# Optimization experiments

Hardware: AMD Instinct MI355X
Metric: run time of the kernel (lower is better)

Reference implementation:

```python
import jax, jax.numpy as jnp
import numpy as np

N = 8192
K = 64
EPS = 1e-7
BN_EPS = 1e-5


def _norm(x):
    return jnp.sqrt(jnp.sum(x * x, axis=-1, keepdims=True))


def _bn(x, gamma, beta):
    # BatchNorm2d in training mode (batch statistics, biased variance)
    mu = jnp.mean(x, axis=(0, 2, 3), keepdims=True)
    var = jnp.mean((x - mu) ** 2, axis=(0, 2, 3), keepdims=True)
    return gamma.reshape(1, -1, 1, 1) * (x - mu) / jnp.sqrt(var + BN_EPS) + beta.reshape(1, -1, 1, 1)


def _conv1x1(x, w, b):
    # 1x1 conv == per-pixel linear: x [B,C,H,W], w [O,C]
    return jnp.einsum('bchw,oc->bohw', x, w) + b.reshape(1, -1, 1, 1)


def setup_inputs() -> dict:
    key = jax.random.key(0)
    ks = jax.random.split(key, 24)
    d = {}
    d['points'] = jax.random.normal(ks[0], (1, N, 3), jnp.float32)
    # graph_conv weights (torch code re-draws these every forward; here fixed params)
    lim0 = float(np.sqrt(6.0 / (4 + 64)))
    d['gw0'] = jax.random.uniform(ks[1], (4, 64), jnp.float32, -lim0, lim0)
    lim = float(np.sqrt(6.0 / (64 + 64)))
    for i in range(1, 5):
        d[f'gw{i}'] = jax.random.uniform(ks[1 + i], (64, 64), jnp.float32, -lim, lim)
    # mlp_1: 4->64->128, mlp_2: 192->256->1024 (1x1 convs + BN)
    d['c1w'] = jax.random.normal(ks[6], (64, 4), jnp.float32) * 0.1
    d['c1b'] = jnp.zeros((64,), jnp.float32)
    d['bn1g'] = jnp.ones((64,), jnp.float32)
    d['bn1b'] = jnp.zeros((64,), jnp.float32)
    d['c2w'] = jax.random.normal(ks[7], (128, 64), jnp.float32) * 0.1
    d['c2b'] = jnp.zeros((128,), jnp.float32)
    d['bn2g'] = jnp.ones((128,), jnp.float32)
    d['bn2b'] = jnp.zeros((128,), jnp.float32)
    d['c3w'] = jax.random.normal(ks[8], (256, 192), jnp.float32) * 0.05
    d['c3b'] = jnp.zeros((256,), jnp.float32)
    d['bn3g'] = jnp.ones((256,), jnp.float32)
    d['bn3b'] = jnp.zeros((256,), jnp.float32)
    d['c4w'] = jax.random.normal(ks[9], (1024, 256), jnp.float32) * 0.05
    d['c4b'] = jnp.zeros((1024,), jnp.float32)
    d['bn4g'] = jnp.ones((1024,), jnp.float32)
    d['bn4b'] = jnp.zeros((1024,), jnp.float32)
    return d


def _knn_search(points, k):
    # pairwise squared distances via ||a||^2 - 2ab + ||b||^2
    r = jnp.sum(points * points, axis=-1, keepdims=True)          # [1,N,1]
    dis = r - 2.0 * jnp.einsum('bnd,bmd->bnm', points, points) + jnp.swapaxes(r, 1, 2)
    _, idx = jax.lax.top_k(-dis, k)                                # [1,N,K]
    knn_pts = jax.vmap(lambda p, i: p[i])(points, idx)             # [1,N,K,3]
    return knn_pts


def _proj_knn(knn_pts):
    b, n, k, _ = knn_pts.shape
    pc = knn_pts - knn_pts[:, :, :1, :]                            # center on first neighbor (self)
    vn = jnp.sqrt(jnp.sum(pc * pc, axis=-1))                       # [1,N,K]
    id1 = jnp.argmax(vn, axis=-1)                                  # farthest neighbor
    a1 = jnp.take_along_axis(pc, jnp.broadcast_to(id1[:, :, None, None], (b, n, 1, 3)), axis=2)[:, :, 0, :]
    a1 = a1 / (_norm(a1) + EPS)
    a2 = jnp.mean(pc, axis=2)
    a2 = a2 / (_norm(a2) + EPS)
    a3 = a1 + 1.5 * a2
    a3 = a3 / (_norm(a3) + EPS)
    den = _norm(pc) + EPS                                          # [1,N,K,1]
    f1 = jnp.sum(pc * a1[:, :, None, :], axis=-1, keepdims=True) / den
    f2 = jnp.sum(pc * a2[:, :, None, :], axis=-1, keepdims=True) / den
    f3 = jnp.sum(pc * a3[:, :, None, :], axis=-1, keepdims=True) / den
    return jnp.concatenate([f1, f2, f3, vn[..., None]], axis=-1)   # [1,N,K,4]


def _proj_points(points):
    b, n, _ = points.shape
    vn = jnp.sqrt(jnp.sum(points * points, axis=-1))               # [1,N]
    i1 = jnp.argmax(vn, axis=-1)
    i2 = jnp.argmin(vn, axis=-1)
    a1 = jnp.take_along_axis(points, jnp.broadcast_to(i1[:, None, None], (b, 1, 3)), axis=1)[:, 0, :]
    a1 = a1 / (_norm(a1) + EPS)
    a2 = jnp.take_along_axis(points, jnp.broadcast_to(i2[:, None, None], (b, 1, 3)), axis=1)[:, 0, :]
    a2 = a2 / (_norm(a2) + EPS)
    a3 = a1 + 1.5 * a2
    a3 = a3 / (_norm(a3) + EPS)
    den = _norm(points) + EPS                                      # [1,N,1]
    f1 = jnp.sum(points * a1[:, None, :], axis=-1, keepdims=True) / den
    f2 = jnp.sum(points * a2[:, None, :], axis=-1, keepdims=True) / den
    f3 = jnp.sum(points * a3[:, None, :], axis=-1, keepdims=True) / den
    return jnp.concatenate([f1, f2, f3, vn[..., None]], axis=-1)   # [1,N,4]


def reference(points, gw0, gw1, gw2, gw3, gw4,
              c1w, c1b, bn1g, bn1b, c2w, c2b, bn2g, bn2b,
              c3w, c3b, bn3g, bn3b, c4w, c4b, bn4g, bn4b):
    n = points.shape[1]
    # upper branch: KNN -> rotation-invariant local feats -> 5-layer MLP -> max over K
    knn_pts = _knn_search(points, K)
    feat_up = _proj_knn(knn_pts)                                   # [1,N,K,4]
    x = feat_up.reshape(-1, 4)
    for w in (gw0, gw1, gw2, gw3, gw4):
        x = jax.nn.relu(x @ w)
    x = x.reshape(1, n, K, 64)
    emb_up = jnp.max(x, axis=2, keepdims=True)                     # [1,N,1,64]
    emb_up = emb_up.reshape(1, 64, n, 1)                           # raw view (reshape), as in torch
    # lower branch: global rotation-invariant feats -> mlp_1
    feat_down = _proj_points(points)                               # [1,N,4]
    emb_down = feat_down.reshape(1, 4, n, 1)                       # raw view (reshape), as in torch
    h = jax.nn.relu(_bn(_conv1x1(emb_down, c1w, c1b), bn1g, bn1b))
    h = jax.nn.relu(_bn(_conv1x1(h, c2w, c2b), bn2g, bn2b))        # [1,128,N,1]
    emb = jnp.concatenate([emb_up, h], axis=1)                     # [1,192,N,1]
    out = jax.nn.relu(_bn(_conv1x1(emb, c3w, c3b), bn3g, bn3b))
    out = jax.nn.relu(_bn(_conv1x1(out, c4w, c4b), bn4g, bn4b))    # [1,1024,N,1]
    return out
```

## Files before the change

### kernel.cpp

```cpp
#include <hip/hip_runtime.h>
#include <hip/hip_bf16.h>

#define NPTS 8192
#define KNN 64
#define EPSF 1e-7f

#define OFF_P4      0
#define OFF_STATS   32768
#define OFF_AVEC    36000
#define OFF_PART    36012
#define OFF_FEATDN  36864
#define OFF_WT1     69632
#define OFF_GWT     69888
#define OFF_BW2     79104
#define OFF_BW3     83200
#define OFF_BW4     107776
#define OFF_XB1     238848
#define OFF_XB3     500992
#define OFF_XB4     1287424
#define OFF_Y1      2336000
#define OFF_Y2      2860288
#define OFF_Y3      3908864
#define OFF_FEATUP  6006016

#define OFF_P4S     OFF_Y1
#define OFF_TBND    (OFF_Y1 + 32768)
#define OFF_BCNT    (OFF_Y1 + 33024)
#define OFF_BOFS    (OFF_Y1 + 33088)
#define OFF_BFIL    (OFF_Y1 + 33156)

typedef __bf16 bf16x8 __attribute__((ext_vector_type(8)));
typedef float  f32x4  __attribute__((ext_vector_type(4)));

__device__ __forceinline__ unsigned f2u(float f) {
    unsigned u = __float_as_uint(f);
    return ((int)u >= 0) ? (u | 0x80000000u) : ~u;
}
__device__ __forceinline__ float key_to_f(unsigned long long k) {
    unsigned v = (unsigned)(k >> 32);
    unsigned ob = (v & 0x80000000u) ? (v ^ 0x80000000u) : ~v;
    return __uint_as_float(ob);
}
__device__ __forceinline__ unsigned short f2bf(float x) {
    unsigned u = __float_as_uint(x);
    unsigned r = (u + 0x7FFFu + ((u >> 16) & 1u)) >> 16;
    return (unsigned short)r;
}
__device__ __forceinline__ unsigned long long u64min(unsigned long long a, unsigned long long b){ return a < b ? a : b; }
__device__ __forceinline__ unsigned long long u64max(unsigned long long a, unsigned long long b){ return a < b ? b : a; }

__device__ __forceinline__ unsigned long long sort_merge(
    unsigned long long key, unsigned long long cur, int lane)
{
    #pragma unroll
    for (int k = 2; k <= 64; k <<= 1) {
        #pragma unroll
        for (int j = k >> 1; j > 0; j >>= 1) {
            unsigned long long o = __shfl_xor(key, j);
            bool up = ((lane & k) == 0);
            bool lower = ((lane & j) == 0);
            key = (lower == up) ? u64min(key, o) : u64max(key, o);
        }
    }
    unsigned long long rev = __shfl(key, 63 - lane);
    unsigned long long m = u64min(cur, rev);
    #pragma unroll
    for (int j = 32; j > 0; j >>= 1) {
        unsigned long long o = __shfl_xor(m, j);
        m = ((lane & j) == 0) ? u64min(m, o) : u64max(m, o);
    }
    return m;
}

__device__ __forceinline__ int xbin(float x) {
    int b = (int)((x + 4.5f) * (64.0f / 9.0f));
    return min(63, max(0, b));
}

__global__ __launch_bounds__(256) void prep_a_kernel(
    const float* __restrict__ points, float* __restrict__ ws)
{
    const int n = blockIdx.x * 256 + threadIdx.x;
    float x = points[3*n+0], y = points[3*n+1], z = points[3*n+2];
    float rr = x*x + y*y + z*z;
    ((float4*)(ws + OFF_P4))[n] = make_float4(x, y, z, rr);
    atomicAdd((int*)(ws + OFF_BCNT) + xbin(x), 1);
    float vn = sqrtf(rr);
    unsigned b = __float_as_uint(vn);
    unsigned long long mxk = ((unsigned long long)b << 32) | (unsigned long long)(0xFFFFFFFFu - (unsigned)n);
    unsigned long long mnk = ((unsigned long long)b << 32) | (unsigned long long)(unsigned)n;
    for (int j = 32; j > 0; j >>= 1) {
        mxk = u64max(mxk, __shfl_xor(mxk, j));
        mnk = u64min(mnk, __shfl_xor(mnk, j));
    }
    __shared__ unsigned long long smx[4], smn[4];
    int wid = threadIdx.x >> 6;
    if ((threadIdx.x & 63) == 0) { smx[wid] = mxk; smn[wid] = mnk; }
    __syncthreads();
    if (threadIdx.x == 0) {
        unsigned long long MX = 0ull, MN = ~0ull;
        for (int i = 0; i < 4; ++i) { MX = u64max(MX, smx[i]); MN = u64min(MN, smn[i]); }
        unsigned long long* parts = (unsigned long long*)(ws + OFF_PART);
        parts[2*blockIdx.x + 0] = MX;
        parts[2*blockIdx.x + 1] = MN;
    }
}

__global__ __launch_bounds__(64) void prep_b_kernel(
    const float* __restrict__ points, float* __restrict__ ws)
{
    const int lane = threadIdx.x;
    const unsigned long long* parts = (const unsigned long long*)(ws + OFF_PART);
    unsigned long long mxk = (lane < 32) ? parts[2*lane + 0] : 0ull;
    unsigned long long mnk = (lane < 32) ? parts[2*lane + 1] : ~0ull;
    for (int j = 32; j > 0; j >>= 1) {
        mxk = u64max(mxk, __shfl_xor(mxk, j));
        mnk = u64min(mnk, __shfl_xor(mnk, j));
    }
    if (lane == 0) {
        int i1 = (int)(0xFFFFFFFFu - (unsigned)(mxk & 0xFFFFFFFFu));
        int i2 = (int)(unsigned)(mnk & 0xFFFFFFFFu);
        float a1x = points[3*i1+0], a1y = points[3*i1+1], a1z = points[3*i1+2];
        float n1 = sqrtf(a1x*a1x + a1y*a1y + a1z*a1z) + EPSF;
        a1x /= n1; a1y /= n1; a1z /= n1;
        float a2x = points[3*i2+0], a2y = points[3*i2+1], a2z = points[3*i2+2];
        float n2 = sqrtf(a2x*a2x + a2y*a2y + a2z*a2z) + EPSF;
        a2x /= n2; a2y /= n2; a2z /= n2;
        float a3x = a1x + 1.5f*a2x, a3y = a1y + 1.5f*a2y, a3z = a1z + 1.5f*a2z;
        float n3 = sqrtf(a3x*a3x + a3y*a3y + a3z*a3z) + EPSF;
        a3x /= n3; a3y /= n3; a3z /= n3;
        float* av = ws + OFF_AVEC;
        av[0]=a1x; av[1]=a1y; av[2]=a1z;
        av[3]=a2x; av[4]=a2y; av[5]=a2z;
        av[6]=a3x; av[7]=a3y; av[8]=a3z;
    }
    if (lane == 1) {
        const int* cnt = (const int*)(ws + OFF_BCNT);
        int* ofs = (int*)(ws + OFF_BOFS);
        int* fil = (int*)(ws + OFF_BFIL);
        int acc = 0;
        for (int i = 0; i < 64; ++i) { ofs[i] = acc; fil[i] = acc; acc += cnt[i]; }
        ofs[64] = acc;
    }
}

__global__ __launch_bounds__(256) void prep_cs_kernel(float* __restrict__ ws)
{
    const int n = blockIdx.x * 256 + threadIdx.x;
    const float* av = ws + OFF_AVEC;
    float4 v = ((const float4*)(ws + OFF_P4))[n];
    float vn = sqrtf(v.w);
    float den = vn + EPSF;
    float f1 = (v.x*av[0] + v.y*av[1] + v.z*av[2]) / den;
    float f2 = (v.x*av[3] + v.y*av[4] + v.z*av[5]) / den;
    float f3 = (v.x*av[6] + v.y*av[7] + v.z*av[8]) / den;
    ((float4*)(ws + OFF_FEATDN))[n] = make_float4(f1, f2, f3, vn);

    int pos = atomicAdd((int*)(ws + OFF_BFIL) + xbin(v.x), 1);
    ((float4*)(ws + OFF_P4S))[pos] = make_float4(v.x, v.y, v.z, __int_as_float(n));
}

__global__ __launch_bounds__(256) void bounds_kernel(float* __restrict__ ws)
{
    const int w = blockIdx.x, tid = threadIdx.x;
    const float4* p = (const float4*)(ws + OFF_P4S);
    float mn = 1e30f, mx = -1e30f;
    #pragma unroll
    for (int i = 0; i < 4; ++i) {
        float x = p[w*1024 + tid + i*256].x;
        mn = fminf(mn, x); mx = fmaxf(mx, x);
    }
    for (int j = 32; j > 0; j >>= 1) {
        mn = fminf(mn, __shfl_xor(mn, j));
        mx = fmaxf(mx, __shfl_xor(mx, j));
    }
    __shared__ float smn[4], smx[4];
    int wid = tid >> 6;
    if ((tid & 63) == 0) { smn[wid] = mn; smx[wid] = mx; }
    __syncthreads();
    if (tid == 0) {
        float MN = fminf(fminf(smn[0], smn[1]), fminf(smn[2], smn[3]));
        float MX = fmaxf(fmaxf(smx[0], smx[1]), fmaxf(smx[2], smx[3]));
        ws[OFF_TBND + 2*w] = MN;
        ws[OFF_TBND + 2*w + 1] = MX;
    }
}

__global__ __launch_bounds__(256) void wt_kernel(
    const float* __restrict__ c1w, const float* __restrict__ c2w,
    const float* __restrict__ c3w, const float* __restrict__ c4w,
    const float* __restrict__ gw0, const float* __restrict__ gw1,
    const float* __restrict__ gw2, const float* __restrict__ gw3,
    const float* __restrict__ gw4,
    float* __restrict__ ws)
{
    const int t = blockIdx.x * 256 + threadIdx.x;
    const int T = gridDim.x * 256;
    for (int m = t; m < 2944; m += T) ws[OFF_STATS + m] = 0.f;
    for (int m = t; m < 64; m += T) ((int*)(ws + OFF_BCNT))[m] = 0;
    for (int m = t; m < 64*4; m += T) { int o = m >> 2, c = m & 3; ws[OFF_WT1 + c*64 + o] = c1w[m]; }

    unsigned short* bw2 = (unsigned short*)(ws + OFF_BW2);
    for (int m = t; m < 128*64; m += T)   bw2[m] = f2bf(c2w[m]);
    unsigned short* bw3 = (unsigned short*)(ws + OFF_BW3);
    for (int m = t; m < 256*192; m += T)  bw3[m] = f2bf(c3w[m]);
    unsigned short* bw4 = (unsigned short*)(ws + OFF_BW4);
    for (int m = t; m < 1024*256; m += T) bw4[m] = f2bf(c4w[m]);

    unsigned short* gwt = (unsigned short*)(ws + OFF_GWT);
    for (int m = t; m < 2048; m += T) {
        int o = m >> 5, i = m & 31;
        gwt[m] = (i < 4) ? f2bf(gw0[i*64 + o]) : (unsigned short)0;
    }
    const float* gsrc[4] = {gw1, gw2, gw3, gw4};
    for (int l = 0; l < 4; ++l) {
        const float* g = gsrc[l];
        unsigned short* dst = gwt + 2048 + l*4096;
        for (int m = t; m < 4096; m += T) { int o = m >> 6, i = m & 63; dst[m] = f2bf(g[i*64 + o]); }
    }
}

__global__ __launch_bounds__(512) void knn_feat_kernel(
    const float4* __restrict__ p4,
    const float4* __restrict__ p4s,
    const float* __restrict__ wbnd,
    float4* __restrict__ feat_up)
{
    __shared__ __align__(16) float4 stage[1024];
    __shared__ unsigned long long queue[8][2][128];
    __shared__ float sb[16], pmx[8], pmn[8];
    __shared__ int voteL, voteR, nextT;

    const int lane = threadIdx.x & 63;
    const int wid  = threadIdx.x >> 6;
    if (threadIdx.x < 16) sb[threadIdx.x] = wbnd[threadIdx.x];
    __syncthreads();
    if (threadIdx.x == 0) {
        float m = -1e30f;
        for (int w = 0; w < 8; ++w) { m = fmaxf(m, sb[2*w+1]); pmx[w] = m; }
        float n = 1e30f;
        for (int w = 7; w >= 0; --w) { n = fminf(n, sb[2*w]); pmn[w] = n; }
    }

    const int s0 = blockIdx.x * 16 + wid * 2;
    float4 qa = p4s[s0];
    float4 qb = p4s[s0 + 1];
    const int qi0 = __float_as_int(qa.w), qi1 = __float_as_int(qb.w);
    qa.w = fmaf(qa.x, qa.x, fmaf(qa.y, qa.y, qa.z * qa.z));
    qb.w = fmaf(qb.x, qb.x, fmaf(qb.y, qb.y, qb.z * qb.z));

    unsigned long long* Q0 = queue[wid][0];
    unsigned long long* Q1 = queue[wid][1];
    unsigned long long cur0 = ~0ull, cur1 = ~0ull;
    float kthd0 = __builtin_inff(), kthd1 = __builtin_inff();
    int qc0 = 0, qc1 = 0;

    const int w0 = blockIdx.x >> 6;
    int L = w0, R = w0, t = w0;

    for (;;) {
        __syncthreads();
        for (int i = threadIdx.x; i < 1024; i += 512) stage[i] = p4s[t*1024 + i];
        if (threadIdx.x == 0) { voteL = 0; voteR = 0; }
        __syncthreads();

        float wmn = sb[2*t], wmx = sb[2*t+1];
        float ga = fmaxf(fmaxf(qa.x - wmx, wmn - qa.x), 0.f);
        float gb = fmaxf(fmaxf(qb.x - wmx, wmn - qb.x), 0.f);
        if (!((ga*ga > kthd0) && (gb*gb > kthd1))) {
            #pragma unroll 2
            for (int sub = 0; sub < 1024; sub += 64) {
                float4 cd = stage[sub + lane];
                int ci = __float_as_int(cd.w);
                float cr = fmaf(cd.x, cd.x, fmaf(cd.y, cd.y, cd.z * cd.z));
                float dot0 = fmaf(qa.x, cd.x, fmaf(qa.y, cd.y, qa.z * cd.z));
                float d0   = fmaf(-2.f, dot0, qa.w) + cr;
                float dot1 = fmaf(qb.x, cd.x, fmaf(qb.y, cd.y, qb.z * cd.z));
                float d1   = fmaf(-2.f, dot1, qb.w) + cr;
                bool p0 = d0 <= kthd0, p1 = d1 <= kthd1;
                unsigned long long m0 = __ballot(p0);
                unsigned long long m1 = __ballot(p1);
                if (m0) {
                    int prefix = __builtin_amdgcn_mbcnt_hi((unsigned)(m0 >> 32),
                                  __builtin_amdgcn_mbcnt_lo((unsigned)m0, 0));
                    if (p0) Q0[qc0 + prefix] = ((unsigned long long)f2u(d0) << 32)
                                             | (unsigned long long)(unsigned)ci;
                    qc0 += __popcll(m0);
                    if (qc0 >= 64) {
                        qc0 -= 64;
                        cur0 = sort_merge(Q0[qc0 + lane], cur0, lane);
                        kthd0 = key_to_f(__shfl(cur0, 63));
                    }
                }
                if (m1) {
                    int prefix = __builtin_amdgcn_mbcnt_hi((unsigned)(m1 >> 32),
                                  __builtin_amdgcn_mbcnt_lo((unsigned)m1, 0));
                    if (p1) Q1[qc1 + prefix] = ((unsigned long long)f2u(d1) << 32)
                                             | (unsigned long long)(unsigned)ci;
                    qc1 += __popcll(m1);
                    if (qc1 >= 64) {
                        qc1 -= 64;
                        cur1 = sort_merge(Q1[qc1 + lane], cur1, lane);
                        kthd1 = key_to_f(__shfl(cur1, 63));
                    }
                }
            }
        }

        if (lane == 0) {
            bool needL = false, needR = false;
            if (L > 0) {
                float p = pmx[L-1];
                float g0 = qa.x - p, g1 = qb.x - p;
                bool st0 = (g0 > 0.f) && (g0*g0 > kthd0);
                bool st1 = (g1 > 0.f) && (g1*g1 > kthd1);
                needL = !(st0 && st1);
            }
            if (R < 7) {
                float p = pmn[R+1];
                float g0 = p - qa.x, g1 = p - qb.x;
                bool st0 = (g0 > 0.f) && (g0*g0 > kthd0);
                bool st1 = (g1 > 0.f) && (g1*g1 > kthd1);
                needR = !(st0 && st1);
            }
            if (needL) atomicOr(&voteL, 1);
            if (needR) atomicOr(&voteR, 1);
        }
        __syncthreads();
        if (threadIdx.x == 0) {
            bool cL = (voteL != 0) && (L > 0);
            bool cR = (voteR != 0) && (R < 7);
            int nt = -1;
            if (cL && cR) nt = ((w0 - (L-1)) <= ((R+1) - w0)) ? (L-1) : (R+1);
            else if (cL) nt = L - 1;
            else if (cR) nt = R + 1;
            nextT = nt;
        }
        __syncthreads();
        t = nextT;
        if (t < 0) break;
        if (t < L) L = t; else R = t;
    }

    cur0 = sort_merge((lane < qc0) ? Q0[lane] : ~0ull, cur0, lane);
    cur1 = sort_merge((lane < qc1) ? Q1[lane] : ~0ull, cur1, lane);

    #pragma unroll 1
    for (int j = 0; j < 2; ++j) {
        unsigned long long cur = j ? cur1 : cur0;
        const int q = j ? qi1 : qi0;
        int nidx = (int)(unsigned)(cur & 0xFFFFFFFFu);
        float4 np = p4[nidx];
        float ox = __shfl(np.x, 0), oy = __shfl(np.y, 0), oz = __shfl(np.z, 0);
        float pcx = np.x - ox, pcy = np.y - oy, pcz = np.z - oz;
        float vn = sqrtf(pcx*pcx + pcy*pcy + pcz*pcz);

        unsigned long long ak = ((unsigned long long)__float_as_uint(vn) << 32)
                              | (unsigned long long)(unsigned)(63 - lane);
        for (int s = 32; s > 0; s >>= 1) ak = u64max(ak, __shfl_xor(ak, s));
        int id1 = 63 - (int)(unsigned)(ak & 0xFFFFFFFFu);

        float a1x = __shfl(pcx, id1), a1y = __shfl(pcy, id1), a1z = __shfl(pcz, id1);
        float n1 = sqrtf(a1x*a1x + a1y*a1y + a1z*a1z) + EPSF;
        a1x /= n1; a1y /= n1; a1z /= n1;

        float sx = pcx, sy = pcy, sz = pcz;
        for (int s = 32; s > 0; s >>= 1) {
            sx += __shfl_xor(sx, s); sy += __shfl_xor(sy, s); sz += __shfl_xor(sz, s);
        }
        float a2x = sx * (1.f/64.f), a2y = sy * (1.f/64.f), a2z = sz * (1.f/64.f);
        float n2 = sqrtf(a2x*a2x + a2y*a2y + a2z*a2z) + EPSF;
        a2x /= n2; a2y /= n2; a2z /= n2;

        float a3x = a1x + 1.5f*a2x, a3y = a1y + 1.5f*a2y, a3z = a1z + 1.5f*a2z;
        float n3 = sqrtf(a3x*a3x + a3y*a3y + a3z*a3z) + EPSF;
        a3x /= n3; a3y /= n3; a3z /= n3;

        float den = vn + EPSF;
        float f1 = (pcx*a1x + pcy*a1y + pcz*a1z) / den;
        float f2 = (pcx*a2x + pcy*a2y + pcz*a2z) / den;
        float f3 = (pcx*a3x + pcy*a3y + pcz*a3z) / den;
        feat_up[q*64 + lane] = make_float4(f1, f2, f3, vn);
    }
}

#define BROW 72
__global__ __launch_bounds__(256) void mlp_kernel(
    const float4* __restrict__ feat_up,
    const unsigned short* __restrict__ gwt,
    unsigned short* __restrict__ xb3)
{
    __shared__ __align__(16) unsigned short Blds[4][64 * BROW];
    const int lane = threadIdx.x & 63;
    const int wid  = threadIdx.x >> 6;
    const int q = blockIdx.x * 4 + wid;
    const int c = lane & 15, g = lane >> 4;
    unsigned short* B = Blds[wid];

    {
        float4 f = feat_up[q*64 + lane];
        uint2 p0;
        p0.x = (unsigned)f2bf(f.x) | ((unsigned)f2bf(f.y) << 16);
        p0.y = (unsigned)f2bf(f.z) | ((unsigned)f2bf(f.w) << 16);
        *(uint2*)&B[lane*BROW] = p0;
        *(uint2*)&B[lane*BROW + 4] = make_uint2(0, 0);
        uint4 z4 = make_uint4(0, 0, 0, 0);
        *(uint4*)&B[lane*BROW + 8]  = z4;
        *(uint4*)&B[lane*BROW + 16] = z4;
        *(uint4*)&B[lane*BROW + 24] = z4;
    }

    const unsigned short* Wl[5] = {gwt, gwt + 2048, gwt + 6144, gwt + 10240, gwt + 14336};
    f32x4 acc[4][4];

    for (int layer = 0; layer < 5; ++layer) {
        const int wstride = (layer == 0) ? 32 : 64;
        const int nks = (layer == 0) ? 1 : 2;
        #pragma unroll
        for (int mb = 0; mb < 4; ++mb)
            #pragma unroll
            for (int nb = 0; nb < 4; ++nb)
                acc[mb][nb] = (f32x4){0.f, 0.f, 0.f, 0.f};

        for (int ks = 0; ks < nks; ++ks) {
            bf16x8 af[4], bf[4];
            #pragma unroll
            for (int mb = 0; mb < 4; ++mb)
                af[mb] = *(const bf16x8*)(Wl[layer] + (mb*16 + c)*wstride + ks*32 + g*8);
            #pragma unroll
            for (int nb = 0; nb < 4; ++nb)
                bf[nb] = *(const bf16x8*)&B[(nb*16 + c)*BROW + ks*32 + g*8];
            #pragma unroll
            for (int mb = 0; mb < 4; ++mb)
                #pragma unroll
                for (int nb = 0; nb < 4; ++nb)
                    acc[mb][nb] = __builtin_amdgcn_mfma_f32_16x16x32_bf16(af[mb], bf[nb], acc[mb][nb], 0, 0, 0);
        }

        if (layer < 4) {
            #pragma unroll
            for (int mb = 0; mb < 4; ++mb) {
                #pragma unroll
                for (int nb = 0; nb < 4; ++nb) {
                    f32x4 a = acc[mb][nb];
                    float r0 = fmaxf(a[0], 0.f), r1 = fmaxf(a[1], 0.f);
                    float r2 = fmaxf(a[2], 0.f), r3 = fmaxf(a[3], 0.f);
                    uint2 pw;
                    pw.x = (unsigned)f2bf(r0) | ((unsigned)f2bf(r1) << 16);
                    pw.y = (unsigned)f2bf(r2) | ((unsigned)f2bf(r3) << 16);
                    *(uint2*)&B[(nb*16 + c)*BROW + mb*16 + g*4] = pw;
                }
            }
        }
    }

    const int cc = q >> 7;
    const int pbase = (q & 127) << 6;
    #pragma unroll
    for (int mb = 0; mb < 4; ++mb) {
        float v[4];
        #pragma unroll
        for (int r = 0; r < 4; ++r)
            v[r] = fmaxf(fmaxf(fmaxf(acc[mb][0][r], acc[mb][1][r]),
                               fmaxf(acc[mb][2][r], acc[mb][3][r])), 0.f);
        #pragma unroll
        for (int mask = 1; mask <= 8; mask <<= 1)
            #pragma unroll
            for (int r = 0; r < 4; ++r)
                v[r] = fmaxf(v[r], __shfl_xor(v[r], mask));
        if (c == 0) {
            #pragma unroll
            for (int r = 0; r < 4; ++r) {
                const int f = mb*16 + g*4 + r;
                xb3[(size_t)(pbase + f) * 192 + cc] = f2bf(v[r]);
            }
        }
    }
}

__global__ __launch_bounds__(256) void conv1_kernel(
    const float* __restrict__ x, const float* __restrict__ wt,
    const float* __restrict__ bias, float* __restrict__ y,
    float* __restrict__ stout)
{
    const int tid = threadIdx.x;
    const int p  = blockIdx.x * 256 + tid;
    const int o0 = blockIdx.y * 32;
    float acc[32];
    #pragma unroll
    for (int u = 0; u < 32; ++u) acc[u] = bias[o0 + u];
    #pragma unroll
    for (int c = 0; c < 4; ++c) {
        float xv = x[c * NPTS + p];
        const float* wr = wt + c * 64 + o0;
        #pragma unroll
        for (int u = 0; u < 32; ++u) acc[u] = fmaf(xv, wr[u], acc[u]);
    }
    #pragma unroll
    for (int u = 0; u < 32; ++u) y[(o0 + u) * NPTS + p] = acc[u];

    __shared__ float ps[4][32], pss[4][32];
    const int wid = tid >> 6, lane = tid & 63;
    #pragma unroll
    for (int u = 0; u < 32; ++u) {
        float s = acc[u], ss = acc[u] * acc[u];
        for (int j = 32; j > 0; j >>= 1) { s += __shfl_xor(s, j); ss += __shfl_xor(ss, j); }
        if (lane == 0) { ps[wid][u] = s; pss[wid][u] = ss; }
    }
    __syncthreads();
    if (tid < 32) {
        float S  = ps[0][tid] + ps[1][tid] + ps[2][tid] + ps[3][tid];
        float SS = pss[0][tid] + pss[1][tid] + pss[2][tid] + pss[3][tid];
        atomicAdd(&stout[o0 + tid], S);
        atomicAdd(&stout[64 + o0 + tid], SS);
    }
}

__global__ __launch_bounds__(256) void bnpack_kernel(
    const float* __restrict__ y, const float* __restrict__ st,
    const float* __restrict__ gam, const float* __restrict__ bet,
    int C, int stride, int coff, unsigned short* __restrict__ xb)
{
    __shared__ float sc[256], sh[256];
    __shared__ __align__(16) unsigned short tile[64][264];
    const int tid = threadIdx.x;
    for (int cc = tid; cc < C; cc += 256) {
        float mu  = st[cc] * (1.f / 8192.f);
        float var = st[C + cc] * (1.f / 8192.f) - mu * mu;
        float s = gam[cc] / sqrtf(var + 1e-5f);
        sc[cc] = s; sh[cc] = bet[cc] - mu * s;
    }
    __syncthreads();
    const int pl = tid & 63, g = tid >> 6;
    const int p = blockIdx.x * 64 + pl;
    for (int c0 = g * 8; c0 < C; c0 += 32) {
        unsigned pk[4];
        #pragma unroll
        for (int h = 0; h < 4; ++h) {
            float v0 = fmaxf(fmaf(y[(c0 + 2*h    ) * NPTS + p], sc[c0 + 2*h    ], sh[c0 + 2*h    ]), 0.f);
            float v1 = fmaxf(fmaf(y[(c0 + 2*h + 1) * NPTS + p], sc[c0 + 2*h + 1], sh[c0 + 2*h + 1]), 0.f);
            pk[h] = (unsigned)f2bf(v0) | ((unsigned)f2bf(v1) << 16);
        }
        *(uint4*)&tile[pl][c0] = make_uint4(pk[0], pk[1], pk[2], pk[3]);
    }
    __syncthreads();
    const int cpr = C >> 3;
    const int nch = 64 * cpr;
    for (int idx = tid; idx < nch; idx += 256) {
        int r = idx / cpr, cc = (idx - r * cpr) * 8;
        *(uint4*)&xb[(size_t)(blockIdx.x * 64 + r) * stride + coff + cc] = *(uint4*)&tile[r][cc];
    }
}

__global__ __launch_bounds__(256) void conv_mfma_kernel(
    const unsigned short* __restrict__ A, const unsigned short* __restrict__ Bx,
    const float* __restrict__ bias, int K, int M,
    float* __restrict__ y, float* __restrict__ stout)
{
    const int lane = threadIdx.x & 63;
    const int w = threadIdx.x >> 6;
    const int n0 = blockIdx.x * 256 + w * 64;
    const int m0 = blockIdx.y * 64;
    const int c = lane & 15, g = lane >> 4;

    f32x4 acc[4][4];
    #pragma unroll
    for (int mt = 0; mt < 4; ++mt)
        #pragma unroll
        for (int nt = 0; nt < 4; ++nt)
            acc[mt][nt] = (f32x4){0.f, 0.f, 0.f, 0.f};

    for (int k0 = 0; k0 < K; k0 += 32) {
        bf16x8 af[4], bf[4];
        #pragma unroll
        for (int mt = 0; mt < 4; ++mt)
            af[mt] = *(const bf16x8*)(A + (size_t)(m0 + mt*16 + c) * K + k0 + g*8);
        #pragma unroll
        for (int nt = 0; nt < 4; ++nt)
            bf[nt] = *(const bf16x8*)(Bx + (size_t)(n0 + nt*16 + c) * K + k0 + g*8);
        #pragma unroll
        for (int mt = 0; mt < 4; ++mt)
            #pragma unroll
            for (int nt = 0; nt < 4; ++nt)
                acc[mt][nt] = __builtin_amdgcn_mfma_f32_16x16x32_bf16(af[mt], bf[nt], acc[mt][nt], 0, 0, 0);
    }

    #pragma unroll
    for (int mt = 0; mt < 4; ++mt) {
        float s[4], ss[4];
        #pragma unroll
        for (int r = 0; r < 4; ++r) {
            const int o = m0 + mt*16 + g*4 + r;
            const float bv = bias[o];
            float sum = 0.f, sq = 0.f;
            #pragma unroll
            for (int nt = 0; nt < 4; ++nt) {
                float v = acc[mt][nt][r] + bv;
                y[(size_t)o * NPTS + n0 + nt*16 + c] = v;
                sum += v; sq += v * v;
            }
            s[r] = sum; ss[r] = sq;
        }
        #pragma unroll
        for (int mask = 1; mask <= 8; mask <<= 1)
            #pragma unroll
            for (int r = 0; r < 4; ++r) {
                s[r]  += __shfl_xor(s[r],  mask);
                ss[r] += __shfl_xor(ss[r], mask);
            }
        if (c == 0) {
            #pragma unroll
            for (int r = 0; r < 4; ++r) {
                const int o = m0 + mt*16 + g*4 + r;
                atomicAdd(&stout[o], s[r]);
                atomicAdd(&stout[M + o], ss[r]);
            }
        }
    }
}

__global__ __launch_bounds__(256) void bnrelu_kernel(
    const float* y, const float* __restrict__ st,
    const float* __restrict__ g, const float* __restrict__ b,
    float* out, int C)
{
    int idx = blockIdx.x * 256 + threadIdx.x;
    int c = idx >> 13;
    float mu  = st[c] * (1.f / 8192.f);
    float var = st[C + c] * (1.f / 8192.f) - mu * mu;
    float scale = g[c] / sqrtf(var + 1e-5f);
    float v = fmaf(y[idx] - mu, scale, b[c]);
    out[idx] = fmaxf(v, 0.f);
}

extern "C" void kernel_launch(void* const* d_in, const int* in_sizes, int n_in,
                              void* d_out, int out_size, void* d_ws, size_t ws_size,
                              hipStream_t stream) {
    const float* points = (const float*)d_in[0];
    const float* gw0 = (const float*)d_in[1];
    const float* gw1 = (const float*)d_in[2];
    const float* gw2 = (const float*)d_in[3];
    const float* gw3 = (const float*)d_in[4];
    const float* gw4 = (const float*)d_in[5];
    const float* c1w = (const float*)d_in[6];  const float* c1b = (const float*)d_in[7];
    const float* bn1g = (const float*)d_in[8]; const float* bn1b = (const float*)d_in[9];
    const float* c2w = (const float*)d_in[10]; const float* c2b = (const float*)d_in[11];
    const float* bn2g = (const float*)d_in[12];const float* bn2b = (const float*)d_in[13];
    const float* c3w = (const float*)d_in[14]; const float* c3b = (const float*)d_in[15];
    const float* bn3g = (const float*)d_in[16];const float* bn3b = (const float*)d_in[17];
    const float* c4w = (const float*)d_in[18]; const float* c4b = (const float*)d_in[19];
    const float* bn4g = (const float*)d_in[20];const float* bn4b = (const float*)d_in[21];

    float* ws = (float*)d_ws;
    float* featdn = ws + OFF_FEATDN;
    float* featup = ws + OFF_FEATUP;
    float* y1 = ws + OFF_Y1; float* y2 = ws + OFF_Y2; float* y3 = ws + OFF_Y3;
    float* s1 = ws + OFF_STATS + 0;
    float* s2 = ws + OFF_STATS + 128;
    float* s3 = ws + OFF_STATS + 384;
    float* s4 = ws + OFF_STATS + 896;
    float* wt1 = ws + OFF_WT1;
    const unsigned short* gwt = (const unsigned short*)(ws + OFF_GWT);
    const unsigned short* bw2 = (const unsigned short*)(ws + OFF_BW2);
    const unsigned short* bw3 = (const unsigned short*)(ws + OFF_BW3);
    const unsigned short* bw4 = (const unsigned short*)(ws + OFF_BW4);
    unsigned short* xb1 = (unsigned short*)(ws + OFF_XB1);
    unsigned short* xb3 = (unsigned short*)(ws + OFF_XB3);
    unsigned short* xb4 = (unsigned short*)(ws + OFF_XB4);
    float* outp = (float*)d_out;

    wt_kernel<<<256, 256, 0, stream>>>(c1w, c2w, c3w, c4w, gw0, gw1, gw2, gw3, gw4, ws);
    prep_a_kernel<<<32, 256, 0, stream>>>(points, ws);
    prep_b_kernel<<<1, 64, 0, stream>>>(points, ws);
    prep_cs_kernel<<<32, 256, 0, stream>>>(ws);
    bounds_kernel<<<8, 256, 0, stream>>>(ws);

    knn_feat_kernel<<<512, 512, 0, stream>>>(
        (const float4*)(ws + OFF_P4), (const float4*)(ws + OFF_P4S),
        ws + OFF_TBND, (float4*)featup);
    mlp_kernel<<<2048, 256, 0, stream>>>((const float4*)featup, gwt, xb3);

    conv1_kernel<<<dim3(32, 2), 256, 0, stream>>>(featdn, wt1, c1b, y1, s1);
    bnpack_kernel<<<128, 256, 0, stream>>>(y1, s1, bn1g, bn1b, 64, 64, 0, xb1);
    conv_mfma_kernel<<<dim3(32, 2), 256, 0, stream>>>(bw2, xb1, c2b, 64, 128, y2, s2);
    bnpack_kernel<<<128, 256, 0, stream>>>(y2, s2, bn2g, bn2b, 128, 192, 64, xb3);
    conv_mfma_kernel<<<dim3(32, 4), 256, 0, stream>>>(bw3, xb3, c3b, 192, 256, y3, s3);
    bnpack_kernel<<<128, 256, 0, stream>>>(y3, s3, bn3g, bn3b, 256, 256, 0, xb4);
    conv_mfma_kernel<<<dim3(32, 16), 256, 0, stream>>>(bw4, xb4, c4b, 256, 1024, outp, s4);
    bnrelu_kernel<<<1024*32, 256, 0, stream>>>(outp, s4, bn4g, bn4b, outp, 1024);
}
```

Measured before the change: 395.7 us.

## Sub-sort KNN tiles by y and prune 64-point chunks with 2D bounds

Adds a kernel that re-sorts each 1024-point x-binned tile by y bins, and records per-64-point y bounds so the KNN search can skip candidate chunks whose combined x/y gap already exceeds both queries' current k-th distances. The KNN kernel is also resized to 256-thread blocks with twice as many blocks. It now writes bf16-packed features directly, which halves the intermediate traffic and removes the conversion from the MLP kernel. This costs one extra small launch and finer-grained branches in the inner loop, and the pruning benefit depends on how the points are distributed.

Result: slower. 441.4 us (+11.6%).

```diff
diff --git a/kernel.cpp b/kernel.cpp
--- a/kernel.cpp
+++ b/kernel.cpp
@@ -25,9 +25,10 @@
 
 #define OFF_P4S     OFF_Y1
 #define OFF_TBND    (OFF_Y1 + 32768)
-#define OFF_BCNT    (OFF_Y1 + 33024)
-#define OFF_BOFS    (OFF_Y1 + 33088)
-#define OFF_BFIL    (OFF_Y1 + 33156)
+#define OFF_SBND    (OFF_Y1 + 32784)
+#define OFF_BCNT    (OFF_Y1 + 33100)
+#define OFF_BOFS    (OFF_Y1 + 33164)
+#define OFF_BFIL    (OFF_Y1 + 33232)
 
 typedef __bf16 bf16x8 __attribute__((ext_vector_type(8)));
 typedef float  f32x4  __attribute__((ext_vector_type(4)));
@@ -72,7 +73,7 @@
     return m;
 }
 
-__device__ __forceinline__ int xbin(float x) {
+__device__ __forceinline__ int bin9(float x) {
     int b = (int)((x + 4.5f) * (64.0f / 9.0f));
     return min(63, max(0, b));
 }
@@ -84,7 +85,7 @@
     float x = points[3*n+0], y = points[3*n+1], z = points[3*n+2];
     float rr = x*x + y*y + z*z;
     ((float4*)(ws + OFF_P4))[n] = make_float4(x, y, z, rr);
-    atomicAdd((int*)(ws + OFF_BCNT) + xbin(x), 1);
+    atomicAdd((int*)(ws + OFF_BCNT) + bin9(x), 1);
     float vn = sqrtf(rr);
     unsigned b = __float_as_uint(vn);
     unsigned long long mxk = ((unsigned long long)b << 32) | (unsigned long long)(0xFFFFFFFFu - (unsigned)n);
@@ -156,31 +157,64 @@
     float f3 = (v.x*av[6] + v.y*av[7] + v.z*av[8]) / den;
     ((float4*)(ws + OFF_FEATDN))[n] = make_float4(f1, f2, f3, vn);
 
-    int pos = atomicAdd((int*)(ws + OFF_BFIL) + xbin(v.x), 1);
+    int pos = atomicAdd((int*)(ws + OFF_BFIL) + bin9(v.x), 1);
     ((float4*)(ws + OFF_P4S))[pos] = make_float4(v.x, v.y, v.z, __int_as_float(n));
+}
+
+__global__ __launch_bounds__(256) void ysort_kernel(float* __restrict__ ws)
+{
+    __shared__ int cnt[64], ofs[64];
+    const int w = blockIdx.x, tid = threadIdx.x;
+    float4* p = (float4*)(ws + OFF_P4S);
+    if (tid < 64) cnt[tid] = 0;
+    __syncthreads();
+    float4 v[4]; int b[4];
+    #pragma unroll
+    for (int i = 0; i < 4; ++i) {
+        v[i] = p[w*1024 + tid + i*256];
+        b[i] = bin9(v[i].y);
+        atomicAdd(&cnt[b[i]], 1);
+    }
+    __syncthreads();
+    if (tid == 0) { int a = 0; for (int i = 0; i < 64; ++i) { ofs[i] = a; a += cnt[i]; } }
+    __syncthreads();
+    #pragma unroll
+    for (int i = 0; i < 4; ++i) {
+        int pos = atomicAdd(&ofs[b[i]], 1);
+        p[w*1024 + pos] = v[i];
+    }
 }
 
 __global__ __launch_bounds__(256) void bounds_kernel(float* __restrict__ ws)
 {
     const int w = blockIdx.x, tid = threadIdx.x;
     const float4* p = (const float4*)(ws + OFF_P4S);
-    float mn = 1e30f, mx = -1e30f;
+    float ymn = 1e30f, ymx = -1e30f, xmn = 1e30f, xmx = -1e30f;
     #pragma unroll
     for (int i = 0; i < 4; ++i) {
-        float x = p[w*1024 + tid + i*256].x;
-        mn = fminf(mn, x); mx = fmaxf(mx, x);
-    }
-    for (int j = 32; j > 0; j >>= 1) {
-        mn = fminf(mn, __shfl_xor(mn, j));
-        mx = fmaxf(mx, __shfl_xor(mx, j));
-    }
-    __shared__ float smn[4], smx[4];
-    int wid = tid >> 6;
-    if ((tid & 63) == 0) { smn[wid] = mn; smx[wid] = mx; }
+        float4 v = p[w*1024 + tid*4 + i];
+        ymn = fminf(ymn, v.y); ymx = fmaxf(ymx, v.y);
+        xmn = fminf(xmn, v.x); xmx = fmaxf(xmx, v.x);
+    }
+    for (int j = 1; j < 16; j <<= 1) {
+        ymn = fminf(ymn, __shfl_xor(ymn, j));
+        ymx = fmaxf(ymx, __shfl_xor(ymx, j));
+    }
+    if ((tid & 15) == 0) {
+        int sub = tid >> 4;
+        ws[OFF_SBND + w*32 + 2*sub]     = ymn;
+        ws[OFF_SBND + w*32 + 2*sub + 1] = ymx;
+    }
+    for (int j = 1; j < 64; j <<= 1) {
+        xmn = fminf(xmn, __shfl_xor(xmn, j));
+        xmx = fmaxf(xmx, __shfl_xor(xmx, j));
+    }
+    __shared__ float sxn[4], sxx[4];
+    if ((tid & 63) == 0) { sxn[tid >> 6] = xmn; sxx[tid >> 6] = xmx; }
     __syncthreads();
     if (tid == 0) {
-        float MN = fminf(fminf(smn[0], smn[1]), fminf(smn[2], smn[3]));
-        float MX = fmaxf(fmaxf(smx[0], smx[1]), fmaxf(smx[2], smx[3]));
+        float MN = fminf(fminf(sxn[0], sxn[1]), fminf(sxn[2], sxn[3]));
+        float MX = fmaxf(fmaxf(sxx[0], sxx[1]), fmaxf(sxx[2], sxx[3]));
         ws[OFF_TBND + 2*w] = MN;
         ws[OFF_TBND + 2*w + 1] = MX;
     }
@@ -220,20 +254,22 @@
     }
 }
 
-__global__ __launch_bounds__(512) void knn_feat_kernel(
+__global__ __launch_bounds__(256) void knn_feat_kernel(
     const float4* __restrict__ p4,
     const float4* __restrict__ p4s,
     const float* __restrict__ wbnd,
-    float4* __restrict__ feat_up)
+    const float* __restrict__ sbnd,
+    uint2* __restrict__ feat_up)
 {
     __shared__ __align__(16) float4 stage[1024];
-    __shared__ unsigned long long queue[8][2][128];
-    __shared__ float sb[16], pmx[8], pmn[8];
+    __shared__ unsigned long long queue[4][2][128];
+    __shared__ float sb[16], sy[256], pmx[8], pmn[8];
     __shared__ int voteL, voteR, nextT;
 
     const int lane = threadIdx.x & 63;
     const int wid  = threadIdx.x >> 6;
-    if (threadIdx.x < 16) sb[threadIdx.x] = wbnd[threadIdx.x];
+    for (int i = threadIdx.x; i < 16; i += 256) sb[i] = wbnd[i];
+    for (int i = threadIdx.x; i < 256; i += 256) sy[i] = sbnd[i];
     __syncthreads();
     if (threadIdx.x == 0) {
         float m = -1e30f;
@@ -242,7 +278,7 @@
         for (int w = 7; w >= 0; --w) { n = fminf(n, sb[2*w]); pmn[w] = n; }
     }
 
-    const int s0 = blockIdx.x * 16 + wid * 2;
+    const int s0 = blockIdx.x * 8 + wid * 2;
     float4 qa = p4s[s0];
     float4 qb = p4s[s0 + 1];
     const int qi0 = __float_as_int(qa.w), qi1 = __float_as_int(qb.w);
@@ -255,22 +291,28 @@
     float kthd0 = __builtin_inff(), kthd1 = __builtin_inff();
     int qc0 = 0, qc1 = 0;
 
-    const int w0 = blockIdx.x >> 6;
+    const int w0 = blockIdx.x >> 7;
     int L = w0, R = w0, t = w0;
 
     for (;;) {
         __syncthreads();
-        for (int i = threadIdx.x; i < 1024; i += 512) stage[i] = p4s[t*1024 + i];
+        for (int i = threadIdx.x; i < 1024; i += 256) stage[i] = p4s[t*1024 + i];
         if (threadIdx.x == 0) { voteL = 0; voteR = 0; }
         __syncthreads();
 
         float wmn = sb[2*t], wmx = sb[2*t+1];
         float ga = fmaxf(fmaxf(qa.x - wmx, wmn - qa.x), 0.f);
         float gb = fmaxf(fmaxf(qb.x - wmx, wmn - qb.x), 0.f);
-        if (!((ga*ga > kthd0) && (gb*gb > kthd1))) {
-            #pragma unroll 2
-            for (int sub = 0; sub < 1024; sub += 64) {
-                float4 cd = stage[sub + lane];
+        float ga2 = ga*ga, gb2 = gb*gb;
+        if (!((ga2 > kthd0) && (gb2 > kthd1))) {
+            #pragma unroll 1
+            for (int sub = 0; sub < 16; ++sub) {
+                float smn = sy[t*32 + 2*sub], smx = sy[t*32 + 2*sub + 1];
+                float gya = fmaxf(fmaxf(qa.y - smx, smn - qa.y), 0.f);
+                float gyb = fmaxf(fmaxf(qb.y - smx, smn - qb.y), 0.f);
+                if ((fmaf(gya, gya, ga2) > kthd0) && (fmaf(gyb, gyb, gb2) > kthd1)) continue;
+
+                float4 cd = stage[sub*64 + lane];
                 int ci = __float_as_int(cd.w);
                 float cr = fmaf(cd.x, cd.x, fmaf(cd.y, cd.y, cd.z * cd.z));
                 float dot0 = fmaf(qa.x, cd.x, fmaf(qa.y, cd.y, qa.z * cd.z));
@@ -364,11 +406,11 @@
         float n1 = sqrtf(a1x*a1x + a1y*a1y + a1z*a1z) + EPSF;
         a1x /= n1; a1y /= n1; a1z /= n1;
 
-        float sx = pcx, sy = pcy, sz = pcz;
+        float sx = pcx, sy2 = pcy, sz = pcz;
         for (int s = 32; s > 0; s >>= 1) {
-            sx += __shfl_xor(sx, s); sy += __shfl_xor(sy, s); sz += __shfl_xor(sz, s);
-        }
-        float a2x = sx * (1.f/64.f), a2y = sy * (1.f/64.f), a2z = sz * (1.f/64.f);
+            sx += __shfl_xor(sx, s); sy2 += __shfl_xor(sy2, s); sz += __shfl_xor(sz, s);
+        }
+        float a2x = sx * (1.f/64.f), a2y = sy2 * (1.f/64.f), a2z = sz * (1.f/64.f);
         float n2 = sqrtf(a2x*a2x + a2y*a2y + a2z*a2z) + EPSF;
         a2x /= n2; a2y /= n2; a2z /= n2;
 
@@ -380,13 +422,16 @@
         float f1 = (pcx*a1x + pcy*a1y + pcz*a1z) / den;
         float f2 = (pcx*a2x + pcy*a2y + pcz*a2z) / den;
         float f3 = (pcx*a3x + pcy*a3y + pcz*a3z) / den;
-        feat_up[q*64 + lane] = make_float4(f1, f2, f3, vn);
+        uint2 pk;
+        pk.x = (unsigned)f2bf(f1) | ((unsigned)f2bf(f2) << 16);
+        pk.y = (unsigned)f2bf(f3) | ((unsigned)f2bf(vn) << 16);
+        feat_up[q*64 + lane] = pk;
     }
 }
 
 #define BROW 72
 __global__ __launch_bounds__(256) void mlp_kernel(
-    const float4* __restrict__ feat_up,
+    const uint2* __restrict__ feat_up,
     const unsigned short* __restrict__ gwt,
     unsigned short* __restrict__ xb3)
 {
@@ -398,10 +443,7 @@
     unsigned short* B = Blds[wid];
 
     {
-        float4 f = feat_up[q*64 + lane];
-        uint2 p0;
-        p0.x = (unsigned)f2bf(f.x) | ((unsigned)f2bf(f.y) << 16);
-        p0.y = (unsigned)f2bf(f.z) | ((unsigned)f2bf(f.w) << 16);
+        uint2 p0 = feat_up[q*64 + lane];
         *(uint2*)&B[lane*BROW] = p0;
         *(uint2*)&B[lane*BROW + 4] = make_uint2(0, 0);
         uint4 z4 = make_uint4(0, 0, 0, 0);
@@ -653,7 +695,6 @@
 
     float* ws = (float*)d_ws;
     float* featdn = ws + OFF_FEATDN;
-    float* featup = ws + OFF_FEATUP;
     float* y1 = ws + OFF_Y1; float* y2 = ws + OFF_Y2; float* y3 = ws + OFF_Y3;
     float* s1 = ws + OFF_STATS + 0;
     float* s2 = ws + OFF_STATS + 128;
@@ -667,18 +708,20 @@
     unsigned short* xb1 = (unsigned short*)(ws + OFF_XB1);
     unsigned short* xb3 = (unsigned short*)(ws + OFF_XB3);
     unsigned short* xb4 = (unsigned short*)(ws + OFF_XB4);
+    uint2* featup = (uint2*)(ws + OFF_FEATUP);
     float* outp = (float*)d_out;
 
     wt_kernel<<<256, 256, 0, stream>>>(c1w, c2w, c3w, c4w, gw0, gw1, gw2, gw3, gw4, ws);
     prep_a_kernel<<<32, 256, 0, stream>>>(points, ws);
     prep_b_kernel<<<1, 64, 0, stream>>>(points, ws);
     prep_cs_kernel<<<32, 256, 0, stream>>>(ws);
+    ysort_kernel<<<8, 256, 0, stream>>>(ws);
     bounds_kernel<<<8, 256, 0, stream>>>(ws);
 
-    knn_feat_kernel<<<512, 512, 0, stream>>>(
+    knn_feat_kernel<<<1024, 256, 0, stream>>>(
         (const float4*)(ws + OFF_P4), (const float4*)(ws + OFF_P4S),
-        ws + OFF_TBND, (float4*)featup);
-    mlp_kernel<<<2048, 256, 0, stream>>>((const float4*)featup, gwt, xb3);
+        ws + OFF_TBND, ws + OFF_SBND, featup);
+    mlp_kernel<<<2048, 256, 0, stream>>>(featup, gwt, xb3);
 
     conv1_kernel<<<dim3(32, 2), 256, 0, stream>>>(featdn, wt1, c1b, y1, s1);
     bnpack_kernel<<<128, 256, 0, stream>>>(y1, s1, bn1g, bn1b, 64, 64, 0, xb1);
```
